# Kernel optimization log

Measured on AMD Instinct MI355X. Metric: run time of the kernel, lower is better.

Reference implementation:

```python
import jax, jax.numpy as jnp
import numpy as np

N_NODES = 100000
N_EDGES = 1200000
D = 64  # in = hid = out = 64


def _seg_sum(vals, idx, n):
    return jax.ops.segment_sum(vals, idx, num_segments=n)


def _graph_conv(x, src, dst, W, b, n_nodes):
    # dgl.nn.GraphConv with norm='both', bias=True:
    #   h = (D_out^-1/2 applied to src feats) -> sum over edges -> D_in^-1/2 -> +b
    # Weight applied first (math-equivalent linear, in==out dims here).
    e = src.shape[0]
    ones = jnp.ones((e,), x.dtype)
    deg_out = jnp.clip(_seg_sum(ones, src, n_nodes), 1.0)  # zero-deg clamp, as in DGL
    deg_in = jnp.clip(_seg_sum(ones, dst, n_nodes), 1.0)
    h = (x @ W) * jax.lax.rsqrt(deg_out)[:, None]          # [N, D]
    agg = _seg_sum(h[src], dst, n_nodes)                   # gather-scatter over edges
    return agg * jax.lax.rsqrt(deg_in)[:, None] + b


def _rgcn(x, edges, params, n_nodes):
    # HeteroGraphConv(aggregate='sum'): sum per-relation GraphConv outputs.
    (s0, d0), (s1, d1) = edges
    h = (_graph_conv(x, s0, d0, params['W1_0'], params['b1_0'], n_nodes)
         + _graph_conv(x, s1, d1, params['W1_1'], params['b1_1'], n_nodes))
    h = jax.nn.relu(h)
    h = (_graph_conv(h, s0, d0, params['W2_0'], params['b2_0'], n_nodes)
         + _graph_conv(h, s1, d1, params['W2_1'], params['b2_1'], n_nodes))
    return h


def setup_inputs() -> dict:
    key = jax.random.key(0)
    ks = jax.random.split(key, 16)
    inp = {
        'x': jax.random.normal(ks[0], (N_NODES, D), dtype=jnp.float32),
        'rel0_src': jax.random.randint(ks[1], (N_EDGES,), 0, N_NODES, dtype=jnp.int32),
        'rel0_dst': jax.random.randint(ks[2], (N_EDGES,), 0, N_NODES, dtype=jnp.int32),
        'rel1_src': jax.random.randint(ks[3], (N_EDGES,), 0, N_NODES, dtype=jnp.int32),
        'rel1_dst': jax.random.randint(ks[4], (N_EDGES,), 0, N_NODES, dtype=jnp.int32),
        'neg_src': jax.random.randint(ks[5], (N_EDGES,), 0, N_NODES, dtype=jnp.int32),
        'neg_dst': jax.random.randint(ks[6], (N_EDGES,), 0, N_NODES, dtype=jnp.int32),
    }
    scale = 1.0 / np.sqrt(D)
    for i, name in enumerate(['W1_0', 'W1_1', 'W2_0', 'W2_1']):
        inp[name] = jax.random.normal(ks[7 + i], (D, D), dtype=jnp.float32) * scale
    for name in ['b1_0', 'b1_1', 'b2_0', 'b2_1']:
        inp[name] = jnp.zeros((D,), dtype=jnp.float32)
    return inp


def reference(x, rel0_src, rel0_dst, rel1_src, rel1_dst, neg_src, neg_dst,
              W1_0, W1_1, W2_0, W2_1, b1_0, b1_1, b2_0, b2_1):
    params = {'W1_0': W1_0, 'b1_0': b1_0, 'W1_1': W1_1, 'b1_1': b1_1,
              'W2_0': W2_0, 'b2_0': b2_0, 'W2_1': W2_1, 'b2_1': b2_1}
    edges = ((rel0_src, rel0_dst), (rel1_src, rel1_dst))
    h = _rgcn(x, edges, params, N_NODES)  # [N, D]
    # HeteroDotProductPredictor: u_dot_v on etype edges -> [E, 1]
    pos_score = jnp.sum(h[rel0_src] * h[rel0_dst], axis=-1, keepdims=True)
    neg_score = jnp.sum(h[neg_src] * h[neg_dst], axis=-1, keepdims=True)
    return pos_score, neg_score
```

## Files before the change

### kernel.cpp

```cpp
#include <hip/hip_runtime.h>
#include <hip/hip_fp16.h>

#define N_NODES 100000
#define N_EDGES 1200000
#define TOTAL_E (2 * N_EDGES)
#define D 64

#define BSH 7
#define NBUCK 782
#define NCHUNK 320
#define CHUNK 7500
#define HIST_L (NBUCK * NCHUNK)
#define HIST2 (2 * HIST_L)
#define SCAN_BS 256
#define SCAN_NB2 ((HIST2 + SCAN_BS - 1) / SCAN_BS)
#define ENT_CAP 4608
#define L2M_GRID ((N_NODES + 127) / 128)
#define NKEY 2048

typedef __attribute__((ext_vector_type(8))) short bf16x8;
typedef __attribute__((ext_vector_type(4))) float f32x4;

__device__ __forceinline__ unsigned short f32_bf16_rne(float f) {
    unsigned u = __float_as_uint(f);
    unsigned r = u + 0x7FFF + ((u >> 16) & 1);
    return (unsigned short)(r >> 16);
}
__device__ __forceinline__ float bf16_f32(unsigned short h) {
    return __uint_as_float(((unsigned)h) << 16);
}

__global__ __launch_bounds__(512) void countA_kernel(const int* __restrict__ s0,
                                                     const int* __restrict__ d0,
                                                     const int* __restrict__ s1,
                                                     const int* __restrict__ d1,
                                                     int* __restrict__ hist) {
    __shared__ int hD[NBUCK];
    __shared__ int hS[NBUCK];
    int t = threadIdx.x;
    for (int i = t; i < NBUCK; i += 512) { hD[i] = 0; hS[i] = 0; }
    __syncthreads();
    int base = blockIdx.x * CHUNK;
    for (int i = t; i < CHUNK; i += 512) {
        int e = base + i;
        int rel = (e >= N_EDGES);
        int src = rel ? s1[e - N_EDGES] : s0[e];
        int dst = rel ? d1[e - N_EDGES] : d0[e];
        atomicAdd(&hD[dst >> BSH], 1);
        atomicAdd(&hS[src >> BSH], 1);
    }
    __syncthreads();
    for (int i = t; i < NBUCK; i += 512) {
        hist[i * NCHUNK + blockIdx.x] = hD[i];
        hist[HIST_L + i * NCHUNK + blockIdx.x] = hS[i];
    }
}

__global__ void scan1_kernel(const int* __restrict__ in, int* __restrict__ out,
                             int* __restrict__ bsum) {
    __shared__ int s[SCAN_BS];
    int t = threadIdx.x;
    int i = blockIdx.x * SCAN_BS + t;
    int v = (i < HIST2) ? in[i] : 0;
    s[t] = v;
    __syncthreads();
    for (int off = 1; off < SCAN_BS; off <<= 1) {
        int add = (t >= off) ? s[t - off] : 0;
        __syncthreads();
        s[t] += add;
        __syncthreads();
    }
    if (i < HIST2) out[i] = s[t] - v;
    if (t == SCAN_BS - 1) bsum[blockIdx.x] = s[t];
}

__global__ void scan2_kernel(int* __restrict__ bsum) {
    __shared__ int s[1024];
    int t = threadIdx.x;
    int v0 = (2 * t < SCAN_NB2) ? bsum[2 * t] : 0;
    int v1 = (2 * t + 1 < SCAN_NB2) ? bsum[2 * t + 1] : 0;
    int sum = v0 + v1;
    s[t] = sum;
    __syncthreads();
    for (int off = 1; off < 1024; off <<= 1) {
        int add = (t >= off) ? s[t - off] : 0;
        __syncthreads();
        s[t] += add;
        __syncthreads();
    }
    int ex = s[t] - sum;
    if (2 * t < SCAN_NB2) bsum[2 * t] = ex;
    if (2 * t + 1 < SCAN_NB2) bsum[2 * t + 1] = ex + v0;
}

__global__ void scan3_kernel(int* __restrict__ out, const int* __restrict__ bsum) {
    int i = blockIdx.x * SCAN_BS + threadIdx.x;
    if (i < HIST2) out[i] += bsum[blockIdx.x];
    if (i == 0) out[HIST2] = 2 * TOTAL_E;
}

__global__ __launch_bounds__(512) void scatterA_kernel(const int* __restrict__ s0,
                                                       const int* __restrict__ d0,
                                                       const int* __restrict__ s1,
                                                       const int* __restrict__ d1,
                                                       const int* __restrict__ OFS,
                                                       unsigned* __restrict__ binned,
                                                       unsigned char* __restrict__ binnedS) {
    __shared__ int cur[NBUCK];
    __shared__ int curS[NBUCK];
    int t = threadIdx.x, wg = blockIdx.x;
    for (int b = t; b < NBUCK; b += 512) {
        cur[b] = OFS[b * NCHUNK + wg];
        curS[b] = OFS[HIST_L + b * NCHUNK + wg] - TOTAL_E;
    }
    __syncthreads();
    int base = wg * CHUNK;
    for (int i = t; i < CHUNK; i += 512) {
        int e = base + i;
        int rel = (e >= N_EDGES);
        int src = rel ? s1[e - N_EDGES] : s0[e];
        int dst = rel ? d1[e - N_EDGES] : d0[e];
        int p = atomicAdd(&cur[dst >> BSH], 1);
        binned[p] = (unsigned)src | ((unsigned)(dst & 127) << 17) | ((unsigned)rel << 24);
        int q = atomicAdd(&curS[src >> BSH], 1);
        binnedS[q] = (unsigned char)((src & 127) | (rel << 7));
    }
}

__global__ __launch_bounds__(512) void sortB_kernel(unsigned* __restrict__ binned,
                                                    const int* __restrict__ OFS,
                                                    int* __restrict__ ip0,
                                                    int* __restrict__ ip1,
                                                    unsigned short* __restrict__ c0a,
                                                    unsigned short* __restrict__ c1a) {
    __shared__ unsigned ent[ENT_CAP];
    __shared__ int cnt[NKEY], pfx[NKEY], cur[NKEY];
    __shared__ int tsum[512];
    int t = threadIdx.x;
    int b = blockIdx.x;
    int start = OFS[b * NCHUNK];
    int end = OFS[(b + 1) * NCHUNK];
    int n = end - start;

    for (int i = t; i < NKEY; i += 512) cnt[i] = 0;
    __syncthreads();
    for (int i = t; i < n; i += 512) {
        unsigned u = binned[start + i];
        if (i < ENT_CAP) ent[i] = u;
        int key = ((int)((u >> 17) & 255) << 3) | (int)((u & 0x1FFFFu) >> 14);
        atomicAdd(&cnt[key], 1);
    }
    __syncthreads();
    int b4 = t * 4;
    int k0 = cnt[b4], k1 = cnt[b4 + 1], k2 = cnt[b4 + 2], k3 = cnt[b4 + 3];
    int s1 = k0 + k1, s2 = s1 + k2, s3 = s2 + k3;
    tsum[t] = s3;
    __syncthreads();
    for (int off = 1; off < 512; off <<= 1) {
        int add = (t >= off) ? tsum[t - off] : 0;
        __syncthreads();
        tsum[t] += add;
        __syncthreads();
    }
    int ex = tsum[t] - s3;
    pfx[b4] = ex;
    pfx[b4 + 1] = ex + k0;
    pfx[b4 + 2] = ex + s1;
    pfx[b4 + 3] = ex + s2;
    cur[b4] = ex;
    cur[b4 + 1] = ex + k0;
    cur[b4 + 2] = ex + s1;
    cur[b4 + 3] = ex + s2;
    __syncthreads();
    for (int i = t; i < n; i += 512) {
        if (i < ENT_CAP) {
            unsigned u = ent[i];
            int key = ((int)((u >> 17) & 255) << 3) | (int)((u & 0x1FFFFu) >> 14);
            int p = atomicAdd(&cur[key], 1);
            binned[start + p] = u & 0x1FFFF;
        }
    }
    if (t < 128) {
        int node = b * 128 + t;
        if (node < N_NODES) {
            int kr0 = t << 3;
            int kr1 = (1 << 10) | (t << 3);
            int p0 = pfx[kr0];
            int e0 = pfx[kr0 + 8];
            int p1 = pfx[kr1];
            int e1 = (t == 127) ? n : pfx[kr1 + 8];
            ip0[node] = start + p0;
            ip1[node] = start + p1;
            c0a[node] = (unsigned short)(e0 - p0);
            c1a[node] = (unsigned short)(e1 - p1);
        }
    }
}

__global__ __launch_bounds__(512) void countO_kernel(const unsigned char* __restrict__ binnedS,
                                                     const int* __restrict__ OFS,
                                                     int* __restrict__ cntO0,
                                                     int* __restrict__ cntO1) {
    __shared__ int cnt[256];
    int t = threadIdx.x;
    int b = blockIdx.x;
    int start = OFS[HIST_L + b * NCHUNK] - TOTAL_E;
    int end = OFS[HIST_L + (b + 1) * NCHUNK] - TOTAL_E;
    if (t < 256) cnt[t] = 0;
    __syncthreads();
    for (int i = start + t; i < end; i += 512)
        atomicAdd(&cnt[(int)binnedS[i]], 1);
    __syncthreads();
    if (t < 128) {
        int node = b * 128 + t;
        if (node < N_NODES) {
            cntO0[node] = cnt[t];
            cntO1[node] = cnt[t | 128];
        }
    }
}

__global__ void wprep_kernel(const float* __restrict__ W0,
                             const float* __restrict__ W1,
                             short* __restrict__ Wf) {
    int t = blockIdx.x * blockDim.x + threadIdx.x;
    if (t >= 2 * 4096) return;
    int rel = t >> 12;
    int e = t & 4095;
    int k = e >> 6, col = e & 63;
    float wv = (rel ? W1 : W0)[e];
    unsigned short hi = f32_bf16_rne(wv);
    unsigned short lo = f32_bf16_rne(wv - bf16_f32(hi));
    int kstep = k >> 5, g = (k >> 3) & 3, j = k & 7;
    int base = ((((rel * 2 + 0) * 2 + kstep) * 4 + g) * 64 + col) * 8 + j;
    int baseL = ((((rel * 2 + 1) * 2 + kstep) * 4 + g) * 64 + col) * 8 + j;
    Wf[base] = (short)hi;
    Wf[baseL] = (short)lo;
}

__global__ __launch_bounds__(256) void lin2m_kernel(const float* __restrict__ x,
                                                    const short* __restrict__ Wf,
                                                    const int* __restrict__ cntO0,
                                                    const int* __restrict__ cntO1,
                                                    __half* __restrict__ y0,
                                                    __half* __restrict__ y1) {
    int t = threadIdx.x;
    int w = t >> 6, lane = t & 63;
    int lr = lane & 15, g = lane >> 4;
    int rowbase = blockIdx.x * 128 + w * 32;

    bf16x8 ah[2][2], al[2][2];
#pragma unroll
    for (int m = 0; m < 2; ++m) {
        int row = rowbase + m * 16 + lr;
        bool ok = row < N_NODES;
        const float* xp = x + (size_t)row * 64 + g * 8;
#pragma unroll
        for (int s = 0; s < 2; ++s) {
            float fv[8];
            if (ok) {
                float4 f0 = ((const float4*)(xp + s * 32))[0];
                float4 f1 = ((const float4*)(xp + s * 32))[1];
                fv[0] = f0.x; fv[1] = f0.y; fv[2] = f0.z; fv[3] = f0.w;
                fv[4] = f1.x; fv[5] = f1.y; fv[6] = f1.z; fv[7] = f1.w;
            } else {
#pragma unroll
                for (int j = 0; j < 8; ++j) fv[j] = 0.f;
            }
#pragma unroll
            for (int j = 0; j < 8; ++j) {
                unsigned short hi = f32_bf16_rne(fv[j]);
                unsigned short lo = f32_bf16_rne(fv[j] - bf16_f32(hi));
                ah[m][s][j] = (short)hi;
                al[m][s][j] = (short)lo;
            }
        }
    }

    float rsc[2][2][4];
#pragma unroll
    for (int m = 0; m < 2; ++m)
#pragma unroll
        for (int reg = 0; reg < 4; ++reg) {
            int row = rowbase + m * 16 + g * 4 + reg;
            bool ok = row < N_NODES;
            rsc[0][m][reg] = ok ? rsqrtf((float)max(cntO0[row], 1)) : 1.f;
            rsc[1][m][reg] = ok ? rsqrtf((float)max(cntO1[row], 1)) : 1.f;
        }

#pragma unroll
    for (int rel = 0; rel < 2; ++rel) {
        __half* yo = rel ? y1 : y0;
        const short* wr = Wf + rel * 8192 + g * 512;
#pragma unroll
        for (int n = 0; n < 4; ++n) {
            const short* wb = wr + (n * 16 + lr) * 8;
            bf16x8 wh0 = *(const bf16x8*)(wb);
            bf16x8 wh1 = *(const bf16x8*)(wb + 2048);
            bf16x8 wl0 = *(const bf16x8*)(wb + 4096);
            bf16x8 wl1 = *(const bf16x8*)(wb + 6144);
#pragma unroll
            for (int m = 0; m < 2; ++m) {
                f32x4 acc = {0.f, 0.f, 0.f, 0.f};
                acc = __builtin_amdgcn_mfma_f32_16x16x32_bf16(al[m][0], wh0, acc, 0, 0, 0);
                acc = __builtin_amdgcn_mfma_f32_16x16x32_bf16(ah[m][0], wl0, acc, 0, 0, 0);
                acc = __builtin_amdgcn_mfma_f32_16x16x32_bf16(ah[m][0], wh0, acc, 0, 0, 0);
                acc = __builtin_amdgcn_mfma_f32_16x16x32_bf16(al[m][1], wh1, acc, 0, 0, 0);
                acc = __builtin_amdgcn_mfma_f32_16x16x32_bf16(ah[m][1], wl1, acc, 0, 0, 0);
                acc = __builtin_amdgcn_mfma_f32_16x16x32_bf16(ah[m][1], wh1, acc, 0, 0, 0);
#pragma unroll
                for (int reg = 0; reg < 4; ++reg) {
                    int row = rowbase + m * 16 + g * 4 + reg;
                    if (row < N_NODES)
                        yo[(size_t)row * 64 + n * 16 + lr] =
                            __float2half_rn(acc[reg] * rsc[rel][m][reg]);
                }
            }
        }
    }
}

template <int RELU, int OUTH>
__global__ __launch_bounds__(256) void aggC_kernel(const __half* __restrict__ L0,
                                                   const __half* __restrict__ L1,
                                                   const unsigned* __restrict__ es,
                                                   const int* __restrict__ ip0,
                                                   const int* __restrict__ ip1,
                                                   const unsigned short* __restrict__ c0a,
                                                   const unsigned short* __restrict__ c1a,
                                                   const float* __restrict__ bia0,
                                                   const float* __restrict__ bia1,
                                                   float* __restrict__ outf,
                                                   __half* __restrict__ outh) {
    int t = threadIdx.x;
    int g = t >> 3, l8 = t & 7;
    int node = blockIdx.x * 32 + g;
    if (node >= N_NODES) return;

    int st0 = ip0[node], c0 = c0a[node];
    int st1 = ip1[node], c1 = c1a[node];

    float a[8] = {0, 0, 0, 0, 0, 0, 0, 0};
    float a2[8] = {0, 0, 0, 0, 0, 0, 0, 0};
    float b[8] = {0, 0, 0, 0, 0, 0, 0, 0};
    float b2[8] = {0, 0, 0, 0, 0, 0, 0, 0};
    union HU { uint4 u; __half2 h[4]; };

    int k = 0;
    for (; k + 2 <= c0; k += 2) {
        int sA = (int)es[st0 + k];
        int sB = (int)es[st0 + k + 1];
        HU uA, uB;
        uA.u = ((const uint4*)(L0 + (size_t)sA * 64))[l8];
        uB.u = ((const uint4*)(L0 + (size_t)sB * 64))[l8];
#pragma unroll
        for (int q = 0; q < 4; ++q) {
            float2 fA = __half22float2(uA.h[q]);
            float2 fB = __half22float2(uB.h[q]);
            a[2 * q] += fA.x;  a[2 * q + 1] += fA.y;
            a2[2 * q] += fB.x; a2[2 * q + 1] += fB.y;
        }
    }
    if (k < c0) {
        int s = (int)es[st0 + k];
        HU uu;
        uu.u = ((const uint4*)(L0 + (size_t)s * 64))[l8];
#pragma unroll
        for (int q = 0; q < 4; ++q) {
            float2 f = __half22float2(uu.h[q]);
            a[2 * q] += f.x;
            a[2 * q + 1] += f.y;
        }
    }
    k = 0;
    for (; k + 2 <= c1; k += 2) {
        int sA = (int)es[st1 + k];
        int sB = (int)es[st1 + k + 1];
        HU uA, uB;
        uA.u = ((const uint4*)(L1 + (size_t)sA * 64))[l8];
        uB.u = ((const uint4*)(L1 + (size_t)sB * 64))[l8];
#pragma unroll
        for (int q = 0; q < 4; ++q) {
            float2 fA = __half22float2(uA.h[q]);
            float2 fB = __half22float2(uB.h[q]);
            b[2 * q] += fA.x;  b[2 * q + 1] += fA.y;
            b2[2 * q] += fB.x; b2[2 * q + 1] += fB.y;
        }
    }
    if (k < c1) {
        int s = (int)es[st1 + k];
        HU uu;
        uu.u = ((const uint4*)(L1 + (size_t)s * 64))[l8];
#pragma unroll
        for (int q = 0; q < 4; ++q) {
            float2 f = __half22float2(uu.h[q]);
            b[2 * q] += f.x;
            b[2 * q + 1] += f.y;
        }
    }

    float r0 = rsqrtf((float)max(c0, 1));
    float r1 = rsqrtf((float)max(c1, 1));
    float4 u0a = ((const float4*)bia0)[l8 * 2];
    float4 u0b = ((const float4*)bia0)[l8 * 2 + 1];
    float4 u1a = ((const float4*)bia1)[l8 * 2];
    float4 u1b = ((const float4*)bia1)[l8 * 2 + 1];
    float o[8];
#pragma unroll
    for (int q = 0; q < 8; ++q) o[q] = (a[q] + a2[q]) * r0 + (b[q] + b2[q]) * r1;
    o[0] += u0a.x + u1a.x; o[1] += u0a.y + u1a.y;
    o[2] += u0a.z + u1a.z; o[3] += u0a.w + u1a.w;
    o[4] += u0b.x + u1b.x; o[5] += u0b.y + u1b.y;
    o[6] += u0b.z + u1b.z; o[7] += u0b.w + u1b.w;
    if (RELU) {
#pragma unroll
        for (int q = 0; q < 8; ++q) o[q] = fmaxf(o[q], 0.f);
    }
    if (OUTH) {
        HU vv;
#pragma unroll
        for (int q = 0; q < 4; ++q)
            vv.h[q] = __floats2half2_rn(o[2 * q], o[2 * q + 1]);
        ((uint4*)(outh + (size_t)node * 64))[l8] = vv.u;
    } else {
        float4 f0 = {o[0], o[1], o[2], o[3]};
        float4 f1 = {o[4], o[5], o[6], o[7]};
        ((float4*)(outf + (size_t)node * 64))[l8 * 2] = f0;
        ((float4*)(outf + (size_t)node * 64))[l8 * 2 + 1] = f1;
    }
}

__global__ __launch_bounds__(256) void score_kernel(const __half* __restrict__ h2,
                                                    const int* __restrict__ ps,
                                                    const int* __restrict__ pd,
                                                    const int* __restrict__ ns,
                                                    const int* __restrict__ nd,
                                                    float* __restrict__ out) {
    int gid = blockIdx.x * blockDim.x + threadIdx.x;
    int pr = gid >> 3;
    int l8 = gid & 7;
    int e0 = pr * 2;
    if (e0 >= TOTAL_E) return;
    int e1 = e0 + 1;
    int sA, dA, sB, dB;
    if (e0 < N_EDGES) { sA = ps[e0]; dA = pd[e0]; sB = ps[e1]; dB = pd[e1]; }
    else {
        sA = ns[e0 - N_EDGES]; dA = nd[e0 - N_EDGES];
        sB = ns[e1 - N_EDGES]; dB = nd[e1 - N_EDGES];
    }
    union HU { uint4 u; __half2 h[4]; };
    HU ua0, ub0, ua1, ub1;
    ua0.u = ((const uint4*)(h2 + (size_t)sA * 64))[l8];
    ub0.u = ((const uint4*)(h2 + (size_t)dA * 64))[l8];
    ua1.u = ((const uint4*)(h2 + (size_t)sB * 64))[l8];
    ub1.u = ((const uint4*)(h2 + (size_t)dB * 64))[l8];
    float p0 = 0.f, p1 = 0.f;
#pragma unroll
    for (int q = 0; q < 4; ++q) {
        float2 fa0 = __half22float2(ua0.h[q]);
        float2 fb0 = __half22float2(ub0.h[q]);
        float2 fa1 = __half22float2(ua1.h[q]);
        float2 fb1 = __half22float2(ub1.h[q]);
        p0 += fa0.x * fb0.x + fa0.y * fb0.y;
        p1 += fa1.x * fb1.x + fa1.y * fb1.y;
    }
    p0 += __shfl_xor(p0, 1);
    p0 += __shfl_xor(p0, 2);
    p0 += __shfl_xor(p0, 4);
    p1 += __shfl_xor(p1, 1);
    p1 += __shfl_xor(p1, 2);
    p1 += __shfl_xor(p1, 4);
    if (l8 == 0) ((float2*)out)[pr] = make_float2(p0, p1);
}

extern "C" void kernel_launch(void* const* d_in, const int* in_sizes, int n_in,
                              void* d_out, int out_size, void* d_ws, size_t ws_size,
                              hipStream_t stream) {
    const float* x    = (const float*)d_in[0];
    const int* s0     = (const int*)d_in[1];
    const int* d0     = (const int*)d_in[2];
    const int* s1     = (const int*)d_in[3];
    const int* d1     = (const int*)d_in[4];
    const int* nsrc   = (const int*)d_in[5];
    const int* ndst   = (const int*)d_in[6];
    const float* W1_0 = (const float*)d_in[7];
    const float* W1_1 = (const float*)d_in[8];
    const float* W2_0 = (const float*)d_in[9];
    const float* W2_1 = (const float*)d_in[10];
    const float* b1_0 = (const float*)d_in[11];
    const float* b1_1 = (const float*)d_in[12];
    const float* b2_0 = (const float*)d_in[13];
    const float* b2_1 = (const float*)d_in[14];
    float* out = (float*)d_out;

    char* p = (char*)d_ws;
    int* cntO0 = (int*)p;      p += N_NODES * 4;
    int* cntO1 = (int*)p;      p += N_NODES * 4;
    int* hist  = (int*)p;      p += (size_t)HIST2 * 4;
    int* OFS   = (int*)p;      p += ((size_t)HIST2 + 8) * 4;
    int* bsum  = (int*)p;      p += 2048 * 4;
    unsigned* binned = (unsigned*)p;  p += (size_t)TOTAL_E * 4;
    int* ip0   = (int*)p;      p += N_NODES * 4;
    int* ip1   = (int*)p;      p += N_NODES * 4;
    unsigned short* c0a = (unsigned short*)p;  p += N_NODES * 2;
    unsigned short* c1a = (unsigned short*)p;  p += N_NODES * 2;
    unsigned char* binnedS = (unsigned char*)p;  p += (size_t)TOTAL_E;
    p = (char*)(((size_t)p + 255) & ~(size_t)255);
    short* WfA = (short*)p;    p += 16384 * 2;
    short* WfB = (short*)p;    p += 16384 * 2;
    p = (char*)(((size_t)p + 255) & ~(size_t)255);
    __half* bufL0h = (__half*)p;  p += (size_t)N_NODES * D * 2;
    __half* bufL1h = (__half*)p;  p += (size_t)N_NODES * D * 2;
    __half* h2h    = (__half*)p;  p += (size_t)N_NODES * D * 2;
    p = (char*)(((size_t)p + 255) & ~(size_t)255);
    float* bufH = (float*)p;   p += (size_t)N_NODES * D * 4;

    const int aggGrid  = (N_NODES + 31) / 32;
    const int scorGrid = (TOTAL_E / 2 * 8 + 255) / 256;

    wprep_kernel<<<32, 256, 0, stream>>>(W1_0, W1_1, WfA);
    wprep_kernel<<<32, 256, 0, stream>>>(W2_0, W2_1, WfB);

    countA_kernel<<<NCHUNK, 512, 0, stream>>>(s0, d0, s1, d1, hist);
    scan1_kernel<<<SCAN_NB2, SCAN_BS, 0, stream>>>(hist, OFS, bsum);
    scan2_kernel<<<1, 1024, 0, stream>>>(bsum);
    scan3_kernel<<<SCAN_NB2, SCAN_BS, 0, stream>>>(OFS, bsum);
    scatterA_kernel<<<NCHUNK, 512, 0, stream>>>(s0, d0, s1, d1, OFS, binned, binnedS);
    sortB_kernel<<<NBUCK, 512, 0, stream>>>(binned, OFS, ip0, ip1, c0a, c1a);
    countO_kernel<<<NBUCK, 512, 0, stream>>>(binnedS, OFS, cntO0, cntO1);

    lin2m_kernel<<<L2M_GRID, 256, 0, stream>>>(x, WfA, cntO0, cntO1, bufL0h, bufL1h);
    aggC_kernel<1, 0><<<aggGrid, 256, 0, stream>>>(bufL0h, bufL1h, binned, ip0, ip1,
                                                   c0a, c1a, b1_0, b1_1, bufH, nullptr);

    lin2m_kernel<<<L2M_GRID, 256, 0, stream>>>(bufH, WfB, cntO0, cntO1, bufL0h, bufL1h);
    aggC_kernel<0, 1><<<aggGrid, 256, 0, stream>>>(bufL0h, bufL1h, binned, ip0, ip1,
                                                   c0a, c1a, b2_0, b2_1, nullptr, h2h);

    score_kernel<<<scorGrid, 256, 0, stream>>>(h2h, s0, d0, nsrc, ndst, out);
}
```

Before: 299.9 us.

## Locally sort edge chunks in LDS before scattering; unroll gather loop by four

The scatter kernel now counts and prefix-sums dst buckets per chunk in shared memory, stages the entries in LDS sorted by bucket, and writes them out in contiguous runs. It repeats the same steps for the src-bucket byte array, so global writes become coalesced instead of random atomically-indexed stores. The aggregation loop also loads four neighbour rows per iteration instead of two, to raise memory-level parallelism. In exchange, the scatter kernel adds many block barriers and LDS use (~40KB), which may lower occupancy.

```diff
diff --git a/kernel.cpp b/kernel.cpp
--- a/kernel.cpp
+++ b/kernel.cpp
@@ -106,24 +106,101 @@
                                                        const int* __restrict__ OFS,
                                                        unsigned* __restrict__ binned,
                                                        unsigned char* __restrict__ binnedS) {
-    __shared__ int cur[NBUCK];
-    __shared__ int curS[NBUCK];
+    __shared__ unsigned ent[CHUNK];
+    __shared__ unsigned short kent[CHUNK];
+    __shared__ int cnt[NBUCK], pfx[NBUCK], cur[NBUCK];
+    __shared__ int tsum[512];
     int t = threadIdx.x, wg = blockIdx.x;
+    int base = wg * CHUNK;
+
+    for (int b = t; b < NBUCK; b += 512) cnt[b] = 0;
+    __syncthreads();
+    for (int i = t; i < CHUNK; i += 512) {
+        int e = base + i;
+        int rel = (e >= N_EDGES);
+        int dst = rel ? d1[e - N_EDGES] : d0[e];
+        atomicAdd(&cnt[dst >> BSH], 1);
+    }
+    __syncthreads();
+    {
+        int b2 = t * 2;
+        int k0 = (b2 < NBUCK) ? cnt[b2] : 0;
+        int k1 = (b2 + 1 < NBUCK) ? cnt[b2 + 1] : 0;
+        int sum = k0 + k1;
+        tsum[t] = sum;
+        __syncthreads();
+        for (int off = 1; off < 512; off <<= 1) {
+            int add = (t >= off) ? tsum[t - off] : 0;
+            __syncthreads();
+            tsum[t] += add;
+            __syncthreads();
+        }
+        int ex = tsum[t] - sum;
+        if (b2 < NBUCK) pfx[b2] = ex;
+        if (b2 + 1 < NBUCK) pfx[b2 + 1] = ex + k0;
+    }
+    __syncthreads();
     for (int b = t; b < NBUCK; b += 512) {
-        cur[b] = OFS[b * NCHUNK + wg];
-        curS[b] = OFS[HIST_L + b * NCHUNK + wg] - TOTAL_E;
-    }
-    __syncthreads();
-    int base = wg * CHUNK;
+        cur[b] = pfx[b];
+        cnt[b] = OFS[b * NCHUNK + wg];
+    }
+    __syncthreads();
     for (int i = t; i < CHUNK; i += 512) {
         int e = base + i;
         int rel = (e >= N_EDGES);
         int src = rel ? s1[e - N_EDGES] : s0[e];
         int dst = rel ? d1[e - N_EDGES] : d0[e];
-        int p = atomicAdd(&cur[dst >> BSH], 1);
-        binned[p] = (unsigned)src | ((unsigned)(dst & 127) << 17) | ((unsigned)rel << 24);
-        int q = atomicAdd(&curS[src >> BSH], 1);
-        binnedS[q] = (unsigned char)((src & 127) | (rel << 7));
+        int kb = dst >> BSH;
+        unsigned u = (unsigned)src | ((unsigned)(dst & 127) << 17) | ((unsigned)rel << 24);
+        int r = atomicAdd(&cur[kb], 1);
+        ent[r] = u;
+        kent[r] = (unsigned short)kb;
+    }
+    __syncthreads();
+    for (int j = t; j < CHUNK; j += 512) {
+        int kb = (int)kent[j];
+        binned[cnt[kb] + (j - pfx[kb])] = ent[j];
+    }
+    __syncthreads();
+    for (int b = t; b < NBUCK; b += 512) cnt[b] = 0;
+    __syncthreads();
+    for (int i = t; i < CHUNK; i += 512)
+        atomicAdd(&cnt[(int)(ent[i] & 0x1FFFFu) >> BSH], 1);
+    __syncthreads();
+    {
+        int b2 = t * 2;
+        int k0 = (b2 < NBUCK) ? cnt[b2] : 0;
+        int k1 = (b2 + 1 < NBUCK) ? cnt[b2 + 1] : 0;
+        int sum = k0 + k1;
+        tsum[t] = sum;
+        __syncthreads();
+        for (int off = 1; off < 512; off <<= 1) {
+            int add = (t >= off) ? tsum[t - off] : 0;
+            __syncthreads();
+            tsum[t] += add;
+            __syncthreads();
+        }
+        int ex = tsum[t] - sum;
+        if (b2 < NBUCK) pfx[b2] = ex;
+        if (b2 + 1 < NBUCK) pfx[b2 + 1] = ex + k0;
+    }
+    __syncthreads();
+    for (int b = t; b < NBUCK; b += 512) {
+        cur[b] = pfx[b];
+        cnt[b] = OFS[HIST_L + b * NCHUNK + wg] - TOTAL_E;
+    }
+    __syncthreads();
+    for (int i = t; i < CHUNK; i += 512) {
+        int kS = (int)(ent[i] & 0x1FFFFu) >> BSH;
+        int r = atomicAdd(&cur[kS], 1);
+        kent[r] = (unsigned short)i;
+    }
+    __syncthreads();
+    for (int j = t; j < CHUNK; j += 512) {
+        unsigned u = ent[(int)kent[j]];
+        int kS = (int)(u & 0x1FFFFu) >> BSH;
+        binnedS[cnt[kS] + (j - pfx[kS])] =
+            (unsigned char)((u & 127) | (((u >> 24) & 1) << 7));
     }
 }
 
@@ -347,21 +424,27 @@
     union HU { uint4 u; __half2 h[4]; };
 
     int k = 0;
-    for (; k + 2 <= c0; k += 2) {
+    for (; k + 4 <= c0; k += 4) {
         int sA = (int)es[st0 + k];
         int sB = (int)es[st0 + k + 1];
-        HU uA, uB;
+        int sC = (int)es[st0 + k + 2];
+        int sD = (int)es[st0 + k + 3];
+        HU uA, uB, uC, uD;
         uA.u = ((const uint4*)(L0 + (size_t)sA * 64))[l8];
         uB.u = ((const uint4*)(L0 + (size_t)sB * 64))[l8];
+        uC.u = ((const uint4*)(L0 + (size_t)sC * 64))[l8];
+        uD.u = ((const uint4*)(L0 + (size_t)sD * 64))[l8];
 #pragma unroll
         for (int q = 0; q < 4; ++q) {
             float2 fA = __half22float2(uA.h[q]);
             float2 fB = __half22float2(uB.h[q]);
-            a[2 * q] += fA.x;  a[2 * q + 1] += fA.y;
-            a2[2 * q] += fB.x; a2[2 * q + 1] += fB.y;
-        }
-    }
-    if (k < c0) {
+            float2 fC = __half22float2(uC.h[q]);
+            float2 fD = __half22float2(uD.h[q]);
+            a[2 * q] += fA.x + fC.x;  a[2 * q + 1] += fA.y + fC.y;
+            a2[2 * q] += fB.x + fD.x; a2[2 * q + 1] += fB.y + fD.y;
+        }
+    }
+    for (; k < c0; ++k) {
         int s = (int)es[st0 + k];
         HU uu;
         uu.u = ((const uint4*)(L0 + (size_t)s * 64))[l8];
@@ -373,21 +456,27 @@
         }
     }
     k = 0;
-    for (; k + 2 <= c1; k += 2) {
+    for (; k + 4 <= c1; k += 4) {
         int sA = (int)es[st1 + k];
         int sB = (int)es[st1 + k + 1];
-        HU uA, uB;
+        int sC = (int)es[st1 + k + 2];
+        int sD = (int)es[st1 + k + 3];
+        HU uA, uB, uC, uD;
         uA.u = ((const uint4*)(L1 + (size_t)sA * 64))[l8];
         uB.u = ((const uint4*)(L1 + (size_t)sB * 64))[l8];
+        uC.u = ((const uint4*)(L1 + (size_t)sC * 64))[l8];
+        uD.u = ((const uint4*)(L1 + (size_t)sD * 64))[l8];
 #pragma unroll
         for (int q = 0; q < 4; ++q) {
             float2 fA = __half22float2(uA.h[q]);
             float2 fB = __half22float2(uB.h[q]);
-            b[2 * q] += fA.x;  b[2 * q + 1] += fA.y;
-            b2[2 * q] += fB.x; b2[2 * q + 1] += fB.y;
-        }
-    }
-    if (k < c1) {
+            float2 fC = __half22float2(uC.h[q]);
+            float2 fD = __half22float2(uD.h[q]);
+            b[2 * q] += fA.x + fC.x;  b[2 * q + 1] += fA.y + fC.y;
+            b2[2 * q] += fB.x + fD.x; b2[2 * q + 1] += fB.y + fD.y;
+        }
+    }
+    for (; k < c1; ++k) {
         int s = (int)es[st1 + k];
         HU uu;
         uu.u = ((const uint4*)(L1 + (size_t)s * 64))[l8];
```

After: 273.3 us. 8.9% less time.
